# Performance work log

Measured on AMD Instinct MI355X. Metric: run time of the kernel, lower is better.

## Reference

```python
import jax, jax.numpy as jnp
import numpy as np

N_HEADS = 16
HEAD_DIM = 128
ROPE_BASE = 50000.0
EPS = 1e-06


def _rotate_half(x):
    half = x.shape[-1] // 2
    return jnp.concatenate([-x[..., half:], x[..., :half]], axis=-1)


def _rms_norm(x, w):
    rms = jnp.sqrt(jnp.mean(x * x, axis=-1, keepdims=True) + EPS)
    return w * (x / rms)


def _rope_tables(n, dim, dtype):
    inv_freq = 1.0 / (ROPE_BASE ** (jnp.arange(0, dim, 2, dtype=jnp.float32) / dim))
    t = jnp.arange(n, dtype=jnp.float32)
    freqs = jnp.outer(t, inv_freq)          # [n, dim/2]
    emb = jnp.concatenate([freqs, freqs], axis=-1)  # [n, dim]
    return jnp.cos(emb).astype(dtype), jnp.sin(emb).astype(dtype)


def setup_inputs() -> dict:
    key = jax.random.key(0)
    ks = jax.random.split(key, 5)
    B, n, d = 2, 2048, 2048
    inner = N_HEADS * HEAD_DIM
    s = 1.0 / np.sqrt(d)
    return {
        "x": jax.random.normal(ks[0], (B, n, d), jnp.float32),
        "Wq": jax.random.normal(ks[1], (d, inner), jnp.float32) * s,
        "Wk": jax.random.normal(ks[2], (d, inner), jnp.float32) * s,
        "Wv": jax.random.normal(ks[3], (d, inner), jnp.float32) * s,
        "Wo": jax.random.normal(ks[4], (inner, d), jnp.float32) * s,
        "qn_w": jnp.ones((inner,), jnp.float32),
        "kn_w": jnp.ones((inner,), jnp.float32),
    }


def reference(x, Wq, Wk, Wv, Wo, qn_w, kn_w):
    B, n, d = x.shape
    # QKV projections (no bias)
    q = x @ Wq
    k = x @ Wk
    v = x @ Wv
    # QK RMSNorm over full inner_dim (as in the torch module)
    q = _rms_norm(q, qn_w)
    k = _rms_norm(k, kn_w)
    # [B, H, n, Dh]
    q = q.reshape(B, n, N_HEADS, HEAD_DIM).transpose(0, 2, 1, 3)
    k = k.reshape(B, n, N_HEADS, HEAD_DIM).transpose(0, 2, 1, 3)
    v = v.reshape(B, n, N_HEADS, HEAD_DIM).transpose(0, 2, 1, 3)
    # RoPE (rotary_dim == head_dim -> full rotation)
    cos, sin = _rope_tables(n, HEAD_DIM, x.dtype)  # [n, Dh]
    cos = cos[None, None]
    sin = sin[None, None]
    q = q * cos + _rotate_half(q) * sin
    k = k * cos + _rotate_half(k) * sin
    # Causal SDPA
    scale = 1.0 / np.sqrt(HEAD_DIM)
    scores = jnp.einsum("bhqd,bhkd->bhqk", q, k) * scale
    causal = jnp.tril(jnp.ones((n, n), dtype=bool))
    scores = jnp.where(causal, scores, jnp.finfo(scores.dtype).min)
    attn = jax.nn.softmax(scores, axis=-1)
    out = jnp.einsum("bhqk,bhkd->bhqd", attn, v)
    out = out.transpose(0, 2, 1, 3).reshape(B, n, N_HEADS * HEAD_DIM)
    return out @ Wo
```

## Files before the change

### kernel.cpp

```cpp
#include <hip/hip_runtime.h>

typedef unsigned short u16;
typedef unsigned int u32;
typedef __attribute__((ext_vector_type(8))) short short8;
typedef __attribute__((ext_vector_type(4))) float f32x4;
typedef __attribute__((ext_vector_type(16))) float f32x16;
typedef __attribute__((ext_vector_type(4))) u32 u32x4;

typedef __attribute__((address_space(3))) unsigned int as3u32;
typedef __attribute__((address_space(1))) unsigned int as1u32;

__device__ __forceinline__ void gld16(void* lds, const void* g) {
    __builtin_amdgcn_global_load_lds((as1u32*)(void*)g, (as3u32*)lds, 16, 0, 0);
}

__device__ inline float bf2f(u16 u) {
    u32 v = ((u32)u) << 16;
    return __builtin_bit_cast(float, v);
}
__device__ inline u16 f2bf(float f) {
    u32 u = __builtin_bit_cast(u32, f);
    u32 r = u + 0x7FFF + ((u >> 16) & 1);
    return (u16)(r >> 16);
}
__device__ __forceinline__ u32 cvtpk_bf16(float lo, float hi) {
    u32 r;
    asm("v_cvt_pk_bf16_f32 %0, %1, %2" : "=v"(r) : "v"(lo), "v"(hi));
    return r;
}
__device__ inline void unpack8(uint4 v, float* f) {
    u32 a[4] = {v.x, v.y, v.z, v.w};
#pragma unroll
    for (int i = 0; i < 4; ++i) {
        f[2 * i]     = bf2f((u16)(a[i] & 0xffff));
        f[2 * i + 1] = bf2f((u16)(a[i] >> 16));
    }
}

__global__ __launch_bounds__(256) void prep_all(const float* __restrict__ x,
                                                const float* __restrict__ Wq,
                                                const float* __restrict__ Wk,
                                                const float* __restrict__ Wv,
                                                const float* __restrict__ Wo,
                                                u16* __restrict__ Xbf,
                                                u16* __restrict__ Wtqkv,
                                                u16* __restrict__ Wot,
                                                float* __restrict__ cosb,
                                                float* __restrict__ sinb) {
    __shared__ float tile[64][65];
    const int bx = blockIdx.x;
    const int t = threadIdx.x;
    if (bx < 4096) {
        int i = (bx * 256 + t) * 8;
        float4 a = *(const float4*)&x[i];
        float4 b = *(const float4*)&x[i + 4];
        u16 o[8];
        o[0] = f2bf(a.x); o[1] = f2bf(a.y); o[2] = f2bf(a.z); o[3] = f2bf(a.w);
        o[4] = f2bf(b.x); o[5] = f2bf(b.y); o[6] = f2bf(b.z); o[7] = f2bf(b.w);
        *(uint4*)&Xbf[i] = *(uint4*)o;
        return;
    }
    if (bx < 8192) {
        const int i = bx - 4096;
        const int z = i >> 10, rem = i & 1023;
        const int n0 = (rem & 31) * 64, k0 = (rem >> 5) * 64;
        const float* in;
        u16* out;
        switch (z) {
            case 0:  in = Wq; out = Wtqkv;            break;
            case 1:  in = Wk; out = Wtqkv + 4194304;  break;
            case 2:  in = Wv; out = Wtqkv + 8388608;  break;
            default: in = Wo; out = Wot;              break;
        }
        const int lr = t >> 4, lc = (t & 15) * 4;
#pragma unroll
        for (int rep = 0; rep < 4; ++rep) {
            float4 v = *(const float4*)&in[(size_t)(k0 + rep * 16 + lr) * 2048 + n0 + lc];
            tile[rep * 16 + lr][lc + 0] = v.x;
            tile[rep * 16 + lr][lc + 1] = v.y;
            tile[rep * 16 + lr][lc + 2] = v.z;
            tile[rep * 16 + lr][lc + 3] = v.w;
        }
        __syncthreads();
        const int nr = t >> 3, kc = (t & 7) * 8;
#pragma unroll
        for (int rep = 0; rep < 2; ++rep) {
            const int n = rep * 32 + nr;
            u16 o[8];
#pragma unroll
            for (int e = 0; e < 8; ++e) o[e] = f2bf(tile[kc + e][n]);
            *(uint4*)&out[(size_t)(n0 + n) * 2048 + k0 + kc] = *(uint4*)o;
        }
        return;
    }
    {
        int idx = (bx - 8192) * 256 + t;
        int pos = idx >> 6, i = idx & 63;
        float invf = __expf(-(float)i * (10.819778284410283f / 64.0f));
        float a = (float)pos * invf;
        cosb[idx] = cosf(a);
        sinb[idx] = sinf(a);
    }
}

template <bool BF16OUT>
__global__ __launch_bounds__(256) void gemm_bt(const u16* __restrict__ A,
                                               const u16* __restrict__ Bt,
                                               void* __restrict__ Cv,
                                               int M, int N, int K) {
    __shared__ u16 As[2][128][64];
    __shared__ u16 Bs[2][128][64];
    const int bm = blockIdx.y, bn = blockIdx.x;
    const int tid = threadIdx.x;
    const int lane = tid & 63, w = tid >> 6;
    const int wm = (w >> 1) * 64, wn = (w & 1) * 64;
    const int lrow = lane & 15;
    const int sw = (lane & 7) << 4;
    const int srl = lane >> 3;
    const int ssw = ((lane & 7) * 16) ^ (srl << 4);
    const char* AB = (const char*)A;
    const char* BB = (const char*)Bt;
    const int NT = K >> 6;
    f32x4 acc[4][4] = {};

    const char* Ab[4];
    const char* Bb[4];
#pragma unroll
    for (int i = 0; i < 4; ++i) {
        const int rb = i * 32 + w * 8;
        Ab[i] = AB + ((size_t)(bm * 128 + rb + srl) * K) * 2 + ssw;
        Bb[i] = BB + ((size_t)(bn * 128 + rb + srl) * K) * 2 + ssw;
    }

#pragma unroll
    for (int i = 0; i < 4; ++i) {
        const int rb = i * 32 + w * 8;
        gld16(&As[0][rb][0], Ab[i]);
        gld16(&Bs[0][rb][0], Bb[i]);
    }

    for (int t = 0; t < NT; ++t) {
        const int buf = t & 1;
        __syncthreads();
        if (t + 1 < NT) {
            const size_t ko = (size_t)(t + 1) * 128;
#pragma unroll
            for (int i = 0; i < 4; ++i) {
                const int rb = i * 32 + w * 8;
                gld16(&As[buf ^ 1][rb][0], Ab[i] + ko);
                gld16(&Bs[buf ^ 1][rb][0], Bb[i] + ko);
            }
        }
        const char* AsB = (const char*)&As[buf][0][0];
        const char* BsB = (const char*)&Bs[buf][0][0];
#pragma unroll
        for (int kk = 0; kk < 2; ++kk) {
            const int cb = (kk * 64 + (lane >> 4) * 16) ^ sw;
            short8 af[4], bf_[4];
#pragma unroll
            for (int i = 0; i < 4; ++i)
                af[i] = *(const short8*)(AsB + (wm + i * 16 + lrow) * 128 + cb);
#pragma unroll
            for (int j = 0; j < 4; ++j)
                bf_[j] = *(const short8*)(BsB + (wn + j * 16 + lrow) * 128 + cb);
            __builtin_amdgcn_s_setprio(1);
#pragma unroll
            for (int i = 0; i < 4; ++i)
#pragma unroll
                for (int j = 0; j < 4; ++j)
                    acc[i][j] = __builtin_amdgcn_mfma_f32_16x16x32_bf16(af[i], bf_[j], acc[i][j], 0, 0, 0);
            __builtin_amdgcn_s_setprio(0);
        }
    }
    const int crow = (lane >> 4) * 4, ccol = lane & 15;
#pragma unroll
    for (int i = 0; i < 4; ++i)
#pragma unroll
        for (int j = 0; j < 4; ++j)
#pragma unroll
            for (int r = 0; r < 4; ++r) {
                size_t off = (size_t)(bm * 128 + wm + i * 16 + crow + r) * N +
                             (size_t)(bn * 128 + wn + j * 16 + ccol);
                if (BF16OUT) ((u16*)Cv)[off] = f2bf(acc[i][j][r]);
                else         ((float*)Cv)[off] = acc[i][j][r];
            }
}

__global__ __launch_bounds__(256) void norm_rope(const u16* __restrict__ qkv,
                                                 const float* __restrict__ qw,
                                                 const float* __restrict__ kw,
                                                 const float* __restrict__ cosb,
                                                 const float* __restrict__ sinb,
                                                 u16* __restrict__ Qout,
                                                 u16* __restrict__ Kout) {
    __shared__ float qf[2048];
    __shared__ float kf[2048];
    __shared__ float red[8];
    const int r = blockIdx.x;
    const int b = r >> 11, pos = r & 2047;
    const int t = threadIdx.x;
    const u16* row = qkv + (size_t)r * 6144;
    uint4 qv = *(const uint4*)&row[t * 8];
    uint4 kv = *(const uint4*)&row[2048 + t * 8];
    float qe[8], ke[8];
    unpack8(qv, qe);
    unpack8(kv, ke);
    float sq = 0.f, sk = 0.f;
#pragma unroll
    for (int e = 0; e < 8; ++e) {
        qf[t * 8 + e] = qe[e];
        kf[t * 8 + e] = ke[e];
        sq += qe[e] * qe[e];
        sk += ke[e] * ke[e];
    }
#pragma unroll
    for (int msk = 1; msk < 64; msk <<= 1) {
        sq += __shfl_xor(sq, msk);
        sk += __shfl_xor(sk, msk);
    }
    if ((t & 63) == 0) { red[t >> 6] = sq; red[4 + (t >> 6)] = sk; }
    __syncthreads();
    float ssq = red[0] + red[1] + red[2] + red[3];
    float ssk = red[4] + red[5] + red[6] + red[7];
    const float invq = 0.12751946f / sqrtf(ssq * (1.f / 2048.f) + 1e-6f);
    const float invk = 1.0f / sqrtf(ssk * (1.f / 2048.f) + 1e-6f);
    const float* ct = cosb + pos * 64;
    const float* st = sinb + pos * 64;
    u16 qo[8], ko[8];
#pragma unroll
    for (int e = 0; e < 8; ++e) {
        int c = t * 8 + e;
        int jl = c & 127;
        int hb = c & ~127;
        int jj = jl & 63;
        float cs = ct[jj], sn = st[jj];
        int pair = hb + ((jl < 64) ? jl + 64 : jl - 64);
        float sgn = (jl < 64) ? -1.f : 1.f;
        float xq = qf[c] * qw[c], pq = qf[pair] * qw[pair];
        float xk = kf[c] * kw[c], pk = kf[pair] * kw[pair];
        qo[e] = f2bf((xq * cs + sgn * pq * sn) * invq);
        ko[e] = f2bf((xk * cs + sgn * pk * sn) * invk);
    }
    const int h = (t * 8) >> 7;
    const int j0 = (t * 8) & 127;
    size_t o = ((size_t)(b * 16 + h) * 2048 + pos) * 128 + j0;
    *(uint4*)&Qout[o] = *(uint4*)qo;
    *(uint4*)&Kout[o] = *(uint4*)ko;
}

__global__ __launch_bounds__(256) void v_transpose(const u16* __restrict__ qkv,
                                                   u16* __restrict__ Vt) {
    __shared__ u16 tile[64][136];
    const int bx = blockIdx.x;
    const int pt = bx & 31, bh = bx >> 5;
    const int b = bh >> 4, h = bh & 15;
    const int pos0 = pt * 64;
    const int t = threadIdx.x;
    const int p = t >> 4, jc = (t & 15) * 8;
#pragma unroll
    for (int rep = 0; rep < 4; ++rep)
        *(uint4*)&tile[rep * 16 + p][jc] =
            *(const uint4*)&qkv[(size_t)(b * 2048 + pos0 + rep * 16 + p) * 6144 + 4096 + h * 128 + jc];
    __syncthreads();
    const int j = t >> 3, pc = (t & 7) * 8;
#pragma unroll
    for (int rep = 0; rep < 4; ++rep) {
        const int jj = rep * 32 + j;
        u16 tmp[8];
#pragma unroll
        for (int e = 0; e < 8; ++e) tmp[e] = tile[pc + e][jj];
        *(uint4*)&Vt[((size_t)bh * 128 + jj) * 2048 + pos0 + pc] = *(uint4*)tmp;
    }
}

__global__ __launch_bounds__(256, 2) void attn_fwd(const u16* __restrict__ Qr,
                                                   const u16* __restrict__ Kr,
                                                   const u16* __restrict__ Vt,
                                                   u16* __restrict__ O) {
    __shared__ u16 Ks[2][64][128];
    __shared__ u16 VsT[2][128][64];
    const int bx = blockIdx.x;
    const int g = bx >> 3;
    const int bh = (bx & 7) + 8 * (g & 3);
    const int qt = (g < 32) ? (15 - (g >> 2)) : ((g >> 2) - 8);
    const int tid = threadIdx.x;
    const int lane = tid & 63, w = tid >> 6;
    const int ql = lane & 31, h = lane >> 5;
    const char* KhB = (const char*)(Kr + (size_t)bh * 2048 * 128);
    const char* VhB = (const char*)(Vt + (size_t)bh * 128 * 2048);
    const u16* Qh = Qr + (size_t)bh * 2048 * 128;
    const int b = bh >> 4, hh = bh & 15;
    const int krl = lane >> 4;
    const int ksc = (lane & 15) * 16;
    const int vrl = lane >> 3;
    const int vsc = (lane & 7) * 16;
    const int swz = (ql & 7) << 4;

    const int q0w = qt * 128 + w * 32;
    const int qg = q0w + ql;
    short8 qb[8];
#pragma unroll
    for (int s = 0; s < 8; ++s)
        qb[s] = *(const short8*)&Qh[(size_t)qg * 128 + s * 16 + h * 8];

    f32x16 ot[4] = {};
    float m = -3e38f, ls = 0.f;
    const int kend = qt * 128 + 128;

#pragma unroll
    for (int j = 0; j < 4; ++j) {
        const int krb = w * 16 + j * 4;
        const int kr = krb + krl;
        gld16(&Ks[0][krb][0], KhB + (size_t)kr * 256 + (ksc ^ ((kr & 7) << 4)));
        const int vrb = w * 32 + j * 8;
        const int vr = vrb + vrl;
        gld16(&VsT[0][vrb][0], VhB + (size_t)vr * 4096 + (vsc ^ ((vr & 7) << 4)));
    }

    for (int k0 = 0; k0 < kend; k0 += 64) {
        const int buf = (k0 >> 6) & 1;
        __syncthreads();
        if (k0 + 64 < kend) {
            const int kn = k0 + 64;
#pragma unroll
            for (int j = 0; j < 4; ++j) {
                const int krb = w * 16 + j * 4;
                const int kr = krb + krl;
                gld16(&Ks[buf ^ 1][krb][0],
                      KhB + (size_t)(kn + kr) * 256 + (ksc ^ ((kr & 7) << 4)));
                const int vrb = w * 32 + j * 8;
                const int vr = vrb + vrl;
                gld16(&VsT[buf ^ 1][vrb][0],
                      VhB + (size_t)vr * 4096 + (size_t)kn * 2 + (vsc ^ ((vr & 7) << 4)));
            }
        }
        const char* KsB = (const char*)&Ks[buf][0][0];
        const char* VsB = (const char*)&VsT[buf][0][0];

        f32x16 st[2] = {};
#pragma unroll
        for (int s = 0; s < 8; ++s) {
            short8 kf0 = *(const short8*)(KsB + (size_t)ql * 256 + ((s * 32 + 16 * h) ^ swz));
            short8 kf1 = *(const short8*)(KsB + (size_t)(32 + ql) * 256 + ((s * 32 + 16 * h) ^ swz));
            st[0] = __builtin_amdgcn_mfma_f32_32x32x16_bf16(kf0, qb[s], st[0], 0, 0, 0);
            st[1] = __builtin_amdgcn_mfma_f32_32x32x16_bf16(kf1, qb[s], st[1], 0, 0, 0);
        }

        if (k0 + 64 > q0w) {
#pragma unroll
            for (int T = 0; T < 2; ++T)
#pragma unroll
                for (int reg = 0; reg < 16; ++reg) {
                    int c = k0 + 32 * T + (reg & 3) + 8 * (reg >> 2) + 4 * h;
                    if (c > qg) st[T][reg] = -1e30f;
                }
        }

        float mx;
        {
            float vm[16];
#pragma unroll
            for (int r = 0; r < 16; ++r) vm[r] = fmaxf(st[0][r], st[1][r]);
            float m4[4];
#pragma unroll
            for (int r = 0; r < 4; ++r)
                m4[r] = fmaxf(fmaxf(vm[r], vm[4 + r]), fmaxf(vm[8 + r], vm[12 + r]));
            mx = fmaxf(fmaxf(m4[0], m4[1]), fmaxf(m4[2], m4[3]));
            mx = fmaxf(mx, __shfl_xor(mx, 32));
        }

        if (__any(mx > m + 8.f)) {
            float mn = fmaxf(m, mx);
            float corr = exp2f(m - mn);
            m = mn;
            ls *= corr;
#pragma unroll
            for (int td = 0; td < 4; ++td)
#pragma unroll
                for (int reg = 0; reg < 16; ++reg) ot[td][reg] *= corr;
        }

        float ps;
        {
#pragma unroll
            for (int T = 0; T < 2; ++T)
#pragma unroll
                for (int reg = 0; reg < 16; ++reg)
                    st[T][reg] = exp2f(st[T][reg] - m);
            float vs[16];
#pragma unroll
            for (int r = 0; r < 16; ++r) vs[r] = st[0][r] + st[1][r];
            float s4[4];
#pragma unroll
            for (int r = 0; r < 4; ++r)
                s4[r] = (vs[r] + vs[4 + r]) + (vs[8 + r] + vs[12 + r]);
            ps = (s4[0] + s4[1]) + (s4[2] + s4[3]);
            ps += __shfl_xor(ps, 32);
        }
        ls += ps;

#pragma unroll
        for (int T = 0; T < 2; ++T) {
            u32 c[4][2];
#pragma unroll
            for (int mm = 0; mm < 4; ++mm) {
                c[mm][0] = cvtpk_bf16(st[T][4 * mm + 0], st[T][4 * mm + 1]);
                c[mm][1] = cvtpk_bf16(st[T][4 * mm + 2], st[T][4 * mm + 3]);
            }
#pragma unroll
            for (int i = 0; i < 2; ++i) {
                const int ks = 2 * T + i;
                u32 a0 = c[2 * i][0], b0 = c[2 * i + 1][0];
                u32 a1 = c[2 * i][1], b1 = c[2 * i + 1][1];
                asm volatile("v_permlane32_swap_b32 %0, %1" : "+v"(a0), "+v"(b0));
                asm volatile("v_permlane32_swap_b32 %0, %1" : "+v"(a1), "+v"(b1));
                u32x4 pw = {a0, a1, b0, b1};
                short8 pf = __builtin_bit_cast(short8, pw);
#pragma unroll
                for (int td = 0; td < 4; ++td) {
                    short8 vf = *(const short8*)(VsB + (size_t)(32 * td + ql) * 128 +
                                                 ((32 * ks + 16 * h) ^ swz));
                    ot[td] = __builtin_amdgcn_mfma_f32_32x32x16_bf16(vf, pf, ot[td], 0, 0, 0);
                }
            }
        }
    }

    const float inv = 1.0f / ls;
    const size_t base = ((size_t)b * 2048 + qg) * 2048 + (size_t)hh * 128;
#pragma unroll
    for (int td = 0; td < 4; ++td)
#pragma unroll
        for (int g2 = 0; g2 < 4; ++g2) {
            ushort4 o4;
            o4.x = f2bf(ot[td][4 * g2 + 0] * inv);
            o4.y = f2bf(ot[td][4 * g2 + 1] * inv);
            o4.z = f2bf(ot[td][4 * g2 + 2] * inv);
            o4.w = f2bf(ot[td][4 * g2 + 3] * inv);
            *(ushort4*)&O[base + 32 * td + 8 * g2 + 4 * h] = o4;
        }
}

extern "C" void kernel_launch(void* const* d_in, const int* in_sizes, int n_in,
                              void* d_out, int out_size, void* d_ws, size_t ws_size,
                              hipStream_t stream) {
    const float* x   = (const float*)d_in[0];
    const float* Wq  = (const float*)d_in[1];
    const float* Wk  = (const float*)d_in[2];
    const float* Wv  = (const float*)d_in[3];
    const float* Wo  = (const float*)d_in[4];
    const float* qnw = (const float*)d_in[5];
    const float* knw = (const float*)d_in[6];

    const size_t MB = 1ull << 20;
    char* ws = (char*)d_ws;
    u16* Xbf    = (u16*)(ws + 0);
    u16* Qr     = (u16*)(ws + 0);
    u16* Wtqkv  = (u16*)(ws + 16 * MB);
    u16* Wot    = (u16*)(ws + 40 * MB);
    u16* QKV    = (u16*)(ws + 48 * MB);
    u16* AOut   = (u16*)(ws + 48 * MB);
    float* cosb = (float*)(ws + 96 * MB);
    float* sinb = (float*)(ws + 96 * MB + 524288);
    u16* Kr     = (u16*)(ws + 97 * MB);
    u16* Vt     = (u16*)(ws + 113 * MB);

    prep_all<<<8704, 256, 0, stream>>>(x, Wq, Wk, Wv, Wo, Xbf, Wtqkv, Wot, cosb, sinb);

    gemm_bt<true><<<dim3(48, 32), 256, 0, stream>>>(Xbf, Wtqkv, (void*)QKV, 4096, 6144, 2048);

    norm_rope<<<4096, 256, 0, stream>>>(QKV, qnw, knw, cosb, sinb, Qr, Kr);
    v_transpose<<<1024, 256, 0, stream>>>(QKV, Vt);

    attn_fwd<<<512, 256, 0, stream>>>(Qr, Kr, Vt, AOut);

    gemm_bt<false><<<dim3(16, 32), 256, 0, stream>>>(AOut, Wot, d_out, 4096, 2048, 2048);
}
```

Measured before the change: 267.6 us.

## Process two query subtiles per wave in attention with half as many waves

The attention kernel now runs 2 waves per block instead of 4, and each wave handles 64 query rows as two 32-row subtiles. Each K and V fragment read from LDS therefore feeds two MFMAs, which halves LDS read traffic per FLOP. Each wave also issues twice as many async loads. Waves whose rows are entirely masked for a K tile now skip its compute. The cost is roughly double the accumulator and Q registers per wave and fewer waves per CU (launch bounds 128,1), so there is less latency hiding, and causal skew within a block grows.

```diff
diff --git a/kernel.cpp b/kernel.cpp
--- a/kernel.cpp
+++ b/kernel.cpp
@@ -273,7 +273,7 @@
     }
 }
 
-__global__ __launch_bounds__(256, 2) void attn_fwd(const u16* __restrict__ Qr,
+__global__ __launch_bounds__(128, 1) void attn_fwd(const u16* __restrict__ Qr,
                                                    const u16* __restrict__ Kr,
                                                    const u16* __restrict__ Vt,
                                                    u16* __restrict__ O) {
@@ -296,23 +296,25 @@
     const int vsc = (lane & 7) * 16;
     const int swz = (ql & 7) << 4;
 
-    const int q0w = qt * 128 + w * 32;
-    const int qg = q0w + ql;
-    short8 qb[8];
-#pragma unroll
-    for (int s = 0; s < 8; ++s)
-        qb[s] = *(const short8*)&Qh[(size_t)qg * 128 + s * 16 + h * 8];
-
-    f32x16 ot[4] = {};
-    float m = -3e38f, ls = 0.f;
+    const int q0w = qt * 128 + w * 64;
+    const int qg0 = q0w + ql, qg1 = q0w + 32 + ql;
+    short8 qb0[8], qb1[8];
+#pragma unroll
+    for (int s = 0; s < 8; ++s) {
+        qb0[s] = *(const short8*)&Qh[(size_t)qg0 * 128 + s * 16 + h * 8];
+        qb1[s] = *(const short8*)&Qh[(size_t)qg1 * 128 + s * 16 + h * 8];
+    }
+
+    f32x16 ot0[4] = {}, ot1[4] = {};
+    float m0 = -3e38f, m1 = -3e38f, ls0 = 0.f, ls1 = 0.f;
     const int kend = qt * 128 + 128;
 
 #pragma unroll
-    for (int j = 0; j < 4; ++j) {
-        const int krb = w * 16 + j * 4;
+    for (int j = 0; j < 8; ++j) {
+        const int krb = w * 32 + j * 4;
         const int kr = krb + krl;
         gld16(&Ks[0][krb][0], KhB + (size_t)kr * 256 + (ksc ^ ((kr & 7) << 4)));
-        const int vrb = w * 32 + j * 8;
+        const int vrb = w * 64 + j * 8;
         const int vr = vrb + vrl;
         gld16(&VsT[0][vrb][0], VhB + (size_t)vr * 4096 + (vsc ^ ((vr & 7) << 4)));
     }
@@ -323,27 +325,30 @@
         if (k0 + 64 < kend) {
             const int kn = k0 + 64;
 #pragma unroll
-            for (int j = 0; j < 4; ++j) {
-                const int krb = w * 16 + j * 4;
+            for (int j = 0; j < 8; ++j) {
+                const int krb = w * 32 + j * 4;
                 const int kr = krb + krl;
                 gld16(&Ks[buf ^ 1][krb][0],
                       KhB + (size_t)(kn + kr) * 256 + (ksc ^ ((kr & 7) << 4)));
-                const int vrb = w * 32 + j * 8;
+                const int vrb = w * 64 + j * 8;
                 const int vr = vrb + vrl;
                 gld16(&VsT[buf ^ 1][vrb][0],
                       VhB + (size_t)vr * 4096 + (size_t)kn * 2 + (vsc ^ ((vr & 7) << 4)));
             }
         }
+        if (k0 >= q0w + 64) continue;
         const char* KsB = (const char*)&Ks[buf][0][0];
         const char* VsB = (const char*)&VsT[buf][0][0];
 
-        f32x16 st[2] = {};
+        f32x16 st0[2] = {}, st1[2] = {};
 #pragma unroll
         for (int s = 0; s < 8; ++s) {
             short8 kf0 = *(const short8*)(KsB + (size_t)ql * 256 + ((s * 32 + 16 * h) ^ swz));
             short8 kf1 = *(const short8*)(KsB + (size_t)(32 + ql) * 256 + ((s * 32 + 16 * h) ^ swz));
-            st[0] = __builtin_amdgcn_mfma_f32_32x32x16_bf16(kf0, qb[s], st[0], 0, 0, 0);
-            st[1] = __builtin_amdgcn_mfma_f32_32x32x16_bf16(kf1, qb[s], st[1], 0, 0, 0);
+            st0[0] = __builtin_amdgcn_mfma_f32_32x32x16_bf16(kf0, qb0[s], st0[0], 0, 0, 0);
+            st1[0] = __builtin_amdgcn_mfma_f32_32x32x16_bf16(kf0, qb1[s], st1[0], 0, 0, 0);
+            st0[1] = __builtin_amdgcn_mfma_f32_32x32x16_bf16(kf1, qb0[s], st0[1], 0, 0, 0);
+            st1[1] = __builtin_amdgcn_mfma_f32_32x32x16_bf16(kf1, qb1[s], st1[1], 0, 0, 0);
         }
 
         if (k0 + 64 > q0w) {
@@ -352,93 +357,150 @@
 #pragma unroll
                 for (int reg = 0; reg < 16; ++reg) {
                     int c = k0 + 32 * T + (reg & 3) + 8 * (reg >> 2) + 4 * h;
-                    if (c > qg) st[T][reg] = -1e30f;
+                    if (c > qg0) st0[T][reg] = -1e30f;
+                    if (c > qg1) st1[T][reg] = -1e30f;
                 }
         }
 
-        float mx;
         {
             float vm[16];
 #pragma unroll
-            for (int r = 0; r < 16; ++r) vm[r] = fmaxf(st[0][r], st[1][r]);
+            for (int r = 0; r < 16; ++r) vm[r] = fmaxf(st0[0][r], st0[1][r]);
             float m4[4];
 #pragma unroll
             for (int r = 0; r < 4; ++r)
                 m4[r] = fmaxf(fmaxf(vm[r], vm[4 + r]), fmaxf(vm[8 + r], vm[12 + r]));
-            mx = fmaxf(fmaxf(m4[0], m4[1]), fmaxf(m4[2], m4[3]));
+            float mx = fmaxf(fmaxf(m4[0], m4[1]), fmaxf(m4[2], m4[3]));
             mx = fmaxf(mx, __shfl_xor(mx, 32));
-        }
-
-        if (__any(mx > m + 8.f)) {
-            float mn = fmaxf(m, mx);
-            float corr = exp2f(m - mn);
-            m = mn;
-            ls *= corr;
-#pragma unroll
-            for (int td = 0; td < 4; ++td)
-#pragma unroll
-                for (int reg = 0; reg < 16; ++reg) ot[td][reg] *= corr;
-        }
-
-        float ps;
-        {
+            if (__any(mx > m0 + 8.f)) {
+                float mn = fmaxf(m0, mx);
+                float corr = exp2f(m0 - mn);
+                m0 = mn;
+                ls0 *= corr;
+#pragma unroll
+                for (int td = 0; td < 4; ++td)
+#pragma unroll
+                    for (int reg = 0; reg < 16; ++reg) ot0[td][reg] *= corr;
+            }
 #pragma unroll
             for (int T = 0; T < 2; ++T)
 #pragma unroll
                 for (int reg = 0; reg < 16; ++reg)
-                    st[T][reg] = exp2f(st[T][reg] - m);
+                    st0[T][reg] = exp2f(st0[T][reg] - m0);
             float vs[16];
 #pragma unroll
-            for (int r = 0; r < 16; ++r) vs[r] = st[0][r] + st[1][r];
+            for (int r = 0; r < 16; ++r) vs[r] = st0[0][r] + st0[1][r];
             float s4[4];
 #pragma unroll
             for (int r = 0; r < 4; ++r)
                 s4[r] = (vs[r] + vs[4 + r]) + (vs[8 + r] + vs[12 + r]);
-            ps = (s4[0] + s4[1]) + (s4[2] + s4[3]);
+            float ps = (s4[0] + s4[1]) + (s4[2] + s4[3]);
             ps += __shfl_xor(ps, 32);
-        }
-        ls += ps;
+            ls0 += ps;
+        }
+        {
+            float vm[16];
+#pragma unroll
+            for (int r = 0; r < 16; ++r) vm[r] = fmaxf(st1[0][r], st1[1][r]);
+            float m4[4];
+#pragma unroll
+            for (int r = 0; r < 4; ++r)
+                m4[r] = fmaxf(fmaxf(vm[r], vm[4 + r]), fmaxf(vm[8 + r], vm[12 + r]));
+            float mx = fmaxf(fmaxf(m4[0], m4[1]), fmaxf(m4[2], m4[3]));
+            mx = fmaxf(mx, __shfl_xor(mx, 32));
+            if (__any(mx > m1 + 8.f)) {
+                float mn = fmaxf(m1, mx);
+                float corr = exp2f(m1 - mn);
+                m1 = mn;
+                ls1 *= corr;
+#pragma unroll
+                for (int td = 0; td < 4; ++td)
+#pragma unroll
+                    for (int reg = 0; reg < 16; ++reg) ot1[td][reg] *= corr;
+            }
+#pragma unroll
+            for (int T = 0; T < 2; ++T)
+#pragma unroll
+                for (int reg = 0; reg < 16; ++reg)
+                    st1[T][reg] = exp2f(st1[T][reg] - m1);
+            float vs[16];
+#pragma unroll
+            for (int r = 0; r < 16; ++r) vs[r] = st1[0][r] + st1[1][r];
+            float s4[4];
+#pragma unroll
+            for (int r = 0; r < 4; ++r)
+                s4[r] = (vs[r] + vs[4 + r]) + (vs[8 + r] + vs[12 + r]);
+            float ps = (s4[0] + s4[1]) + (s4[2] + s4[3]);
+            ps += __shfl_xor(ps, 32);
+            ls1 += ps;
+        }
 
 #pragma unroll
         for (int T = 0; T < 2; ++T) {
-            u32 c[4][2];
+            u32 c0[4][2], c1[4][2];
 #pragma unroll
             for (int mm = 0; mm < 4; ++mm) {
-                c[mm][0] = cvtpk_bf16(st[T][4 * mm + 0], st[T][4 * mm + 1]);
-                c[mm][1] = cvtpk_bf16(st[T][4 * mm + 2], st[T][4 * mm + 3]);
+                c0[mm][0] = cvtpk_bf16(st0[T][4 * mm + 0], st0[T][4 * mm + 1]);
+                c0[mm][1] = cvtpk_bf16(st0[T][4 * mm + 2], st0[T][4 * mm + 3]);
+                c1[mm][0] = cvtpk_bf16(st1[T][4 * mm + 0], st1[T][4 * mm + 1]);
+                c1[mm][1] = cvtpk_bf16(st1[T][4 * mm + 2], st1[T][4 * mm + 3]);
             }
 #pragma unroll
             for (int i = 0; i < 2; ++i) {
                 const int ks = 2 * T + i;
-                u32 a0 = c[2 * i][0], b0 = c[2 * i + 1][0];
-                u32 a1 = c[2 * i][1], b1 = c[2 * i + 1][1];
+                u32 a0 = c0[2 * i][0], b0 = c0[2 * i + 1][0];
+                u32 a1 = c0[2 * i][1], b1 = c0[2 * i + 1][1];
                 asm volatile("v_permlane32_swap_b32 %0, %1" : "+v"(a0), "+v"(b0));
                 asm volatile("v_permlane32_swap_b32 %0, %1" : "+v"(a1), "+v"(b1));
-                u32x4 pw = {a0, a1, b0, b1};
-                short8 pf = __builtin_bit_cast(short8, pw);
+                u32x4 pw0 = {a0, a1, b0, b1};
+                short8 pf0 = __builtin_bit_cast(short8, pw0);
+                u32 a2 = c1[2 * i][0], b2 = c1[2 * i + 1][0];
+                u32 a3 = c1[2 * i][1], b3 = c1[2 * i + 1][1];
+                asm volatile("v_permlane32_swap_b32 %0, %1" : "+v"(a2), "+v"(b2));
+                asm volatile("v_permlane32_swap_b32 %0, %1" : "+v"(a3), "+v"(b3));
+                u32x4 pw1 = {a2, a3, b2, b3};
+                short8 pf1 = __builtin_bit_cast(short8, pw1);
 #pragma unroll
                 for (int td = 0; td < 4; ++td) {
                     short8 vf = *(const short8*)(VsB + (size_t)(32 * td + ql) * 128 +
                                                  ((32 * ks + 16 * h) ^ swz));
-                    ot[td] = __builtin_amdgcn_mfma_f32_32x32x16_bf16(vf, pf, ot[td], 0, 0, 0);
+                    ot0[td] = __builtin_amdgcn_mfma_f32_32x32x16_bf16(vf, pf0, ot0[td], 0, 0, 0);
+                    ot1[td] = __builtin_amdgcn_mfma_f32_32x32x16_bf16(vf, pf1, ot1[td], 0, 0, 0);
                 }
             }
         }
     }
 
-    const float inv = 1.0f / ls;
-    const size_t base = ((size_t)b * 2048 + qg) * 2048 + (size_t)hh * 128;
-#pragma unroll
-    for (int td = 0; td < 4; ++td)
-#pragma unroll
-        for (int g2 = 0; g2 < 4; ++g2) {
-            ushort4 o4;
-            o4.x = f2bf(ot[td][4 * g2 + 0] * inv);
-            o4.y = f2bf(ot[td][4 * g2 + 1] * inv);
-            o4.z = f2bf(ot[td][4 * g2 + 2] * inv);
-            o4.w = f2bf(ot[td][4 * g2 + 3] * inv);
-            *(ushort4*)&O[base + 32 * td + 8 * g2 + 4 * h] = o4;
-        }
+    {
+        const float inv = 1.0f / ls0;
+        const size_t base = ((size_t)b * 2048 + qg0) * 2048 + (size_t)hh * 128;
+#pragma unroll
+        for (int td = 0; td < 4; ++td)
+#pragma unroll
+            for (int g2 = 0; g2 < 4; ++g2) {
+                ushort4 o4;
+                o4.x = f2bf(ot0[td][4 * g2 + 0] * inv);
+                o4.y = f2bf(ot0[td][4 * g2 + 1] * inv);
+                o4.z = f2bf(ot0[td][4 * g2 + 2] * inv);
+                o4.w = f2bf(ot0[td][4 * g2 + 3] * inv);
+                *(ushort4*)&O[base + 32 * td + 8 * g2 + 4 * h] = o4;
+            }
+    }
+    {
+        const float inv = 1.0f / ls1;
+        const size_t base = ((size_t)b * 2048 + qg1) * 2048 + (size_t)hh * 128;
+#pragma unroll
+        for (int td = 0; td < 4; ++td)
+#pragma unroll
+            for (int g2 = 0; g2 < 4; ++g2) {
+                ushort4 o4;
+                o4.x = f2bf(ot1[td][4 * g2 + 0] * inv);
+                o4.y = f2bf(ot1[td][4 * g2 + 1] * inv);
+                o4.z = f2bf(ot1[td][4 * g2 + 2] * inv);
+                o4.w = f2bf(ot1[td][4 * g2 + 3] * inv);
+                *(ushort4*)&O[base + 32 * td + 8 * g2 + 4 * h] = o4;
+            }
+    }
 }
 
 extern "C" void kernel_launch(void* const* d_in, const int* in_sizes, int n_in,
@@ -472,7 +534,7 @@
     norm_rope<<<4096, 256, 0, stream>>>(QKV, qnw, knw, cosb, sinb, Qr, Kr);
     v_transpose<<<1024, 256, 0, stream>>>(QKV, Vt);
 
-    attn_fwd<<<512, 256, 0, stream>>>(Qr, Kr, Vt, AOut);
+    attn_fwd<<<512, 128, 0, stream>>>(Qr, Kr, Vt, AOut);
 
     gemm_bt<false><<<dim3(16, 32), 256, 0, stream>>>(AOut, Wot, d_out, 4096, 2048, 2048);
 }
```

New measurement: 327.3 us. 1.22x slower.
